# Kernel optimization log

Measured on AMD Instinct MI355X. Metric: run time of the kernel, lower is better.

The kernel has to match this reference:

```python
import jax, jax.numpy as jnp
import numpy as np

N_NODES = 50000
N_EDGES = 800000
HIDDEN = 256
LAYERS = 10


def setup_inputs() -> dict:
    key = jax.random.key(0)
    ks = jax.random.split(key, 8)
    x = jax.random.normal(ks[0], (N_NODES, 1), dtype=jnp.float32)
    edge_index = jax.random.randint(ks[1], (2, N_EDGES), 0, N_NODES, dtype=jnp.int64)
    # GCNConv weights (Glorot-ish scale)
    W1 = jax.random.normal(ks[2], (1, HIDDEN), dtype=jnp.float32) * (1.0 / np.sqrt(1))
    b1 = jnp.zeros((HIDDEN,), dtype=jnp.float32)
    W = jax.random.normal(ks[3], (HIDDEN, HIDDEN), dtype=jnp.float32) * (1.0 / np.sqrt(HIDDEN))
    b = jnp.zeros((HIDDEN,), dtype=jnp.float32)
    Wc = jax.random.normal(ks[4], (HIDDEN, 1), dtype=jnp.float32) * (1.0 / np.sqrt(HIDDEN))
    bc = jnp.zeros((1,), dtype=jnp.float32)
    return {"x": x, "edge_index": edge_index, "W1": W1, "b1": b1,
            "W": W, "b": b, "Wc": Wc, "bc": bc}


def _gcn_norm(edge_index, n_nodes):
    # PyG GCNConv default: add self-loops, symmetric normalization
    loop = jnp.arange(n_nodes, dtype=edge_index.dtype)
    src = jnp.concatenate([edge_index[0], loop])
    dst = jnp.concatenate([edge_index[1], loop])
    ones = jnp.ones(src.shape[0], dtype=jnp.float32)
    deg = jax.ops.segment_sum(ones, dst, num_segments=n_nodes)
    dinv = jnp.where(deg > 0, jax.lax.rsqrt(deg), 0.0)
    norm = dinv[src] * dinv[dst]  # [E+N]
    return src, dst, norm


def _gcn_conv(h, W, b, src, dst, norm, n_nodes):
    h = h @ W                                   # [N, H] dense transform first (small GEMM)
    msg = h[src] * norm[:, None]                # gather + scale  [E+N, H]
    out = jax.ops.segment_sum(msg, dst, num_segments=n_nodes)  # scatter-add
    return out + b


def reference(x, edge_index, W1, b1, W, b, Wc, bc):
    n = x.shape[0]
    src, dst, norm = _gcn_norm(edge_index, n)  # graph is static across layers
    h = jax.nn.relu(_gcn_conv(x, W1, b1, src, dst, norm, n))
    for _ in range(1, LAYERS):  # layers 1..9 share the same weights (self.conv reused)
        h = jax.nn.relu(_gcn_conv(h, W, b, src, dst, norm, n))
    return h @ Wc + bc  # [N, 1]
```

## Files before the change

### kernel.cpp

```cpp
#include <hip/hip_runtime.h>

typedef long long ll;
typedef __attribute__((ext_vector_type(8))) short short8;
typedef __attribute__((ext_vector_type(4))) float f32x4;
constexpr int HID = 256;
constexpr int LDSS = 264;

__device__ inline ushort f2bf(float f){
  uint u = __float_as_uint(f);
  u += 0x7FFFu + ((u >> 16) & 1u);
  return (ushort)(u >> 16);
}

__device__ inline int pinv(int q){ return (q & ~63) | ((q & 3)*16 + ((q >> 2) & 15)); }

__global__ void k_diag(float* out, int n, float val){
  int i = blockIdx.x*256 + threadIdx.x;
  if (i < n) out[i] = val;
}

__global__ void k_detect(const int* ei, int* flag){
  __shared__ int bad;
  if (threadIdx.x == 0) bad = 0;
  __syncthreads();
  for (int i = threadIdx.x; i < 2048; i += 256)
    if (ei[2*i+1] != 0) bad = 1;
  __syncthreads();
  if (threadIdx.x == 0) *flag = bad ? 0 : 1;
}

__global__ void k_count(const int* ei, ll E, const int* flag, int* cnt){
  ll i = (ll)blockIdx.x*256 + threadIdx.x;
  if (i >= E) return;
  int f = *flag;
  int d = f ? (int)((const ll*)ei)[E + i] : ei[E + i];
  atomicAdd(&cnt[d], 1);
}

__global__ void k_scan_a(const int* __restrict__ cnt, int* __restrict__ bsum, int n){
  __shared__ int s[256];
  int t = threadIdx.x, i = blockIdx.x*256 + t;
  s[t] = (i < n) ? cnt[i] : 0;
  __syncthreads();
  for (int off = 128; off; off >>= 1){
    if (t < off) s[t] += s[t + off];
    __syncthreads();
  }
  if (t == 0) bsum[blockIdx.x] = s[0];
}

__global__ void k_scan_b(const int* __restrict__ bsum, int* __restrict__ boff,
                         int nb, int* __restrict__ row_ptr, int n){
  __shared__ int s[256];
  int t = threadIdx.x;
  int v = (t < nb) ? bsum[t] : 0;
  s[t] = v; __syncthreads();
  for (int off = 1; off < 256; off <<= 1){
    int add = (t >= off) ? s[t - off] : 0;
    __syncthreads();
    s[t] += add;
    __syncthreads();
  }
  if (t < nb) boff[t] = s[t] - v;
  if (t == nb - 1) row_ptr[n] = s[t];
}

__global__ void k_scan_c(const int* __restrict__ cnt, const int* __restrict__ boff,
                         int* __restrict__ row_ptr, const float* __restrict__ x,
                         float* __restrict__ dinv, float* __restrict__ xd, int n){
  __shared__ int s[256];
  int t = threadIdx.x, i = blockIdx.x*256 + t;
  int v = (i < n) ? cnt[i] : 0;
  s[t] = v; __syncthreads();
  for (int off = 1; off < 256; off <<= 1){
    int add = (t >= off) ? s[t - off] : 0;
    __syncthreads();
    s[t] += add;
    __syncthreads();
  }
  if (i < n){
    row_ptr[i] = boff[blockIdx.x] + s[t] - v;
    float dv = 1.0f / sqrtf((float)(v + 1));
    dinv[i] = dv;
    xd[i] = x[i] * dv;
  }
}

__global__ void k_place(const int* ei, ll E, const int* flag, int* fill, int* col){
  ll i = (ll)blockIdx.x*256 + threadIdx.x;
  if (i >= E) return;
  int f = *flag;
  int s, d;
  if (f){ const ll* e64 = (const ll*)ei; s = (int)e64[i]; d = (int)e64[E + i]; }
  else  { s = ei[i]; d = ei[E + i]; }
  int p = atomicAdd(&fill[d], 1);
  col[p] = s;
}

__global__ void k_layer1(const float* __restrict__ xd, const int* __restrict__ row_ptr,
                         const int* __restrict__ col, float* __restrict__ g, int n){
  int i = blockIdx.x*256 + threadIdx.x;
  if (i >= n) return;
  float s = xd[i];
  int e0 = row_ptr[i], e1 = row_ptr[i+1];
  for (int e = e0; e < e1; ++e) s += xd[col[e]];
  g[i] = s;
}

__global__ void k_prep(const float* __restrict__ W, short* __restrict__ Bt,
                       const float* b1, const float* W1, const float* bm, const float* Wc,
                       float* b1_p, float* W1_p, float* bm_p, float* Wc_p){
  int idx = blockIdx.x*256 + threadIdx.x;
  if (idx < 16*8*64){
    int nb = idx >> 9, kc = (idx >> 6) & 7, l = idx & 63;
    short8 hi;
    #pragma unroll
    for (int j = 0; j < 8; ++j){
      int k = pinv(kc*32 + ((l >> 4) * 8) + j);
      int c = nb*16 + (l & 15);
      hi[j] = (short)f2bf(W[k*HID + c]);
    }
    ((short8*)Bt)[idx] = hi;
  } else if (blockIdx.x == 32){
    int q = threadIdx.x;
    int c = pinv(q);
    b1_p[q] = b1[c];
    W1_p[q] = W1[c];
    bm_p[q] = bm[c];
    Wc_p[q] = Wc[c];
  }
}

template<int MODE>
__global__ __launch_bounds__(256, 4) void k_gemm_mfma(
  const void* __restrict__ Ain, const short* __restrict__ Bt,
  const float* __restrict__ bias, const float* __restrict__ W1,
  const float* __restrict__ dinv, ushort* __restrict__ ts_bf, int n)
{
  __shared__ short Ah[64*LDSS];
  int t = threadIdx.x;
  int r0 = blockIdx.x * 64;

  #pragma unroll
  for (int i = 0; i < 8; ++i){
    int id  = i*256 + t;
    int row = id >> 5;
    int c16 = id & 31;
    int v   = r0 + row;
    short8 hi8 = {0,0,0,0,0,0,0,0};
    if (v < n){
      if (MODE == 0){
        float gv = dinv[v] * ((const float*)Ain)[v];
        const float4* wp = (const float4*)(W1 + c16*8);
        const float4* bp = (const float4*)(bias + c16*8);
        float4 w0 = wp[0], w1 = wp[1], b0 = bp[0], b1 = bp[1];
        hi8[0] = (short)f2bf(fmaxf(fmaf(gv,w0.x,b0.x), 0.f));
        hi8[1] = (short)f2bf(fmaxf(fmaf(gv,w0.y,b0.y), 0.f));
        hi8[2] = (short)f2bf(fmaxf(fmaf(gv,w0.z,b0.z), 0.f));
        hi8[3] = (short)f2bf(fmaxf(fmaf(gv,w0.w,b0.w), 0.f));
        hi8[4] = (short)f2bf(fmaxf(fmaf(gv,w1.x,b1.x), 0.f));
        hi8[5] = (short)f2bf(fmaxf(fmaf(gv,w1.y,b1.y), 0.f));
        hi8[6] = (short)f2bf(fmaxf(fmaf(gv,w1.z,b1.z), 0.f));
        hi8[7] = (short)f2bf(fmaxf(fmaf(gv,w1.w,b1.w), 0.f));
      } else {
        hi8 = ((const short8*)Ain)[(size_t)v*32 + c16];
      }
    }
    *(short8*)&Ah[row*LDSS + c16*8] = hi8;
  }
  __syncthreads();

  int l = t & 63, w = t >> 6;
  const short8* Btv = (const short8*)Bt;
  f32x4 acc[4][4];
  #pragma unroll
  for (int m = 0; m < 4; ++m)
    #pragma unroll
    for (int nf = 0; nf < 4; ++nf)
      acc[m][nf] = (f32x4){0.f,0.f,0.f,0.f};

  for (int kc = 0; kc < 8; ++kc){
    short8 ah[4];
    #pragma unroll
    for (int m = 0; m < 4; ++m){
      int row = m*16 + (l & 15);
      ah[m] = *(const short8*)&Ah[row*LDSS + (kc*4 + (l >> 4))*8];
    }
    #pragma unroll
    for (int nf = 0; nf < 4; ++nf){
      int nb = w*4 + nf;
      short8 bh = Btv[(size_t)(nb*8 + kc)*64 + l];
      #pragma unroll
      for (int m = 0; m < 4; ++m){
        acc[m][nf] = __builtin_amdgcn_mfma_f32_16x16x32_bf16(ah[m], bh, acc[m][nf], 0,0,0);
      }
    }
  }

  #pragma unroll
  for (int m = 0; m < 4; ++m){
    #pragma unroll
    for (int r = 0; r < 4; ++r){
      int v = r0 + m*16 + ((l >> 4)*4) + r;
      if (v < n){
        float dv = dinv[v];
        uint2 o;
        o.x = (uint)f2bf(dv * acc[m][0][r]) | ((uint)f2bf(dv * acc[m][1][r]) << 16);
        o.y = (uint)f2bf(dv * acc[m][2][r]) | ((uint)f2bf(dv * acc[m][3][r]) << 16);
        *(uint2*)((char*)ts_bf + (size_t)v*512 + w*128 + (l & 15)*8) = o;
      }
    }
  }
}

__device__ inline void bfacc(uint2 u, float4& a){
  a.x += __uint_as_float(u.x << 16);
  a.y += __uint_as_float(u.x & 0xFFFF0000u);
  a.z += __uint_as_float(u.y << 16);
  a.w += __uint_as_float(u.y & 0xFFFF0000u);
}

template<int LAST>
__global__ __launch_bounds__(256, 4) void k_scatter_bf(
  const ushort* __restrict__ ts_bf, const int* __restrict__ row_ptr,
  const int* __restrict__ col, const float* __restrict__ bias,
  const float* __restrict__ dinv, ushort* __restrict__ Abf,
  const float* __restrict__ Wc, const float* __restrict__ bc,
  float* __restrict__ out, int n)
{
  int w = (int)((blockIdx.x*256 + threadIdx.x) >> 6);
  int lane = threadIdx.x & 63;
  if (w >= n) return;
  const uint2* tsp = ((const uint2*)ts_bf) + lane;
  int e0 = row_ptr[w], e1 = row_ptr[w+1];

  float4 a0 = make_float4(0.f,0.f,0.f,0.f);
  float4 a1 = make_float4(0.f,0.f,0.f,0.f);
  float4 a2 = make_float4(0.f,0.f,0.f,0.f);
  float4 a3 = make_float4(0.f,0.f,0.f,0.f);
  bfacc(tsp[(size_t)w*64], a0);

  int e = e0;
  for (; e + 4 <= e1; e += 4){
    int c0 = __builtin_nontemporal_load(col + e + 0);
    int c1 = __builtin_nontemporal_load(col + e + 1);
    int c2 = __builtin_nontemporal_load(col + e + 2);
    int c3 = __builtin_nontemporal_load(col + e + 3);
    uint2 v0 = tsp[(size_t)c0*64];
    uint2 v1 = tsp[(size_t)c1*64];
    uint2 v2 = tsp[(size_t)c2*64];
    uint2 v3 = tsp[(size_t)c3*64];
    bfacc(v0, a0); bfacc(v1, a1); bfacc(v2, a2); bfacc(v3, a3);
  }
  for (; e < e1; ++e){
    uint2 v = tsp[(size_t)__builtin_nontemporal_load(col + e)*64];
    bfacc(v, a0);
  }

  a0.x += a1.x + a2.x + a3.x;
  a0.y += a1.y + a2.y + a3.y;
  a0.z += a1.z + a2.z + a3.z;
  a0.w += a1.w + a2.w + a3.w;

  float dv = dinv[w];
  float4 bb = ((const float4*)bias)[lane];
  if (LAST == 0){
    uint2 o;
    o.x = (uint)f2bf(fmaxf(fmaf(dv, a0.x, bb.x), 0.f))
        | ((uint)f2bf(fmaxf(fmaf(dv, a0.y, bb.y), 0.f)) << 16);
    o.y = (uint)f2bf(fmaxf(fmaf(dv, a0.z, bb.z), 0.f))
        | ((uint)f2bf(fmaxf(fmaf(dv, a0.w, bb.w), 0.f)) << 16);
    ((uint2*)Abf)[(size_t)w*64 + lane] = o;
  } else {
    float4 wc = ((const float4*)Wc)[lane];
    float s = fmaxf(fmaf(dv, a0.x, bb.x), 0.f)*wc.x
            + fmaxf(fmaf(dv, a0.y, bb.y), 0.f)*wc.y
            + fmaxf(fmaf(dv, a0.z, bb.z), 0.f)*wc.z
            + fmaxf(fmaf(dv, a0.w, bb.w), 0.f)*wc.w;
    #pragma unroll
    for (int off = 32; off; off >>= 1) s += __shfl_down(s, off, 64);
    if (lane == 0) out[w] = s + bc[0];
  }
}

extern "C" void kernel_launch(void* const* d_in, const int* in_sizes, int n_in,
                              void* d_out, int out_size, void* d_ws, size_t ws_size,
                              hipStream_t stream)
{
  const float* x  = (const float*)d_in[0];
  const int*   ei = (const int*)d_in[1];
  const float* W1 = (const float*)d_in[2];
  const float* b1 = (const float*)d_in[3];
  const float* Wm = (const float*)d_in[4];
  const float* bm = (const float*)d_in[5];
  const float* Wc = (const float*)d_in[6];
  const float* bc = (const float*)d_in[7];
  float* out = (float*)d_out;
  const int N = in_sizes[0];
  const ll  E = in_sizes[1] / 2;

  char* ws = (char*)d_ws;
  size_t off = 0;
  auto carve = [&](size_t bytes)->char*{
    char* p = ws + off; off += (bytes + 255) & ~(size_t)255; return p;
  };
  int*   cnt     = (int*)  carve((size_t)N*4);
  int*   row_ptr = (int*)  carve((size_t)(N+1)*4);
  int*   fill    = (int*)  carve((size_t)N*4);
  float* dinv    = (float*)carve((size_t)N*4);
  float* xd      = (float*)carve((size_t)N*4);
  float* g       = (float*)carve((size_t)N*4);
  int*   flag    = (int*)  carve(256);
  int*   bsum    = (int*)  carve(1024);
  int*   boff    = (int*)  carve(1024);
  float* b1_p    = (float*)carve(1024);
  float* W1_p    = (float*)carve(1024);
  float* bm_p    = (float*)carve(1024);
  float* Wc_p    = (float*)carve(1024);
  short* Bt      = (short*)carve((size_t)8192*8*2);
  int*   col     = (int*)  carve((size_t)E*4);
  ushort* ts_bf  = (ushort*)carve((size_t)N*HID*2);
  ushort* Abf    = (ushort*)carve((size_t)N*HID*2);
  if (off > ws_size){
    k_diag<<<(out_size+255)/256, 256, 0, stream>>>(out, out_size, (float)(ws_size >> 20));
    return;
  }

  hipMemsetAsync(cnt, 0, (size_t)N*4, stream);
  k_detect<<<1, 256, 0, stream>>>(ei, flag);
  int eblocks = (int)((E + 255) / 256);
  k_count<<<eblocks, 256, 0, stream>>>(ei, E, flag, cnt);
  int nb = (N + 255) / 256;
  k_scan_a<<<nb, 256, 0, stream>>>(cnt, bsum, N);
  k_scan_b<<<1, 256, 0, stream>>>(bsum, boff, nb, row_ptr, N);
  k_scan_c<<<nb, 256, 0, stream>>>(cnt, boff, row_ptr, x, dinv, xd, N);
  hipMemcpyAsync(fill, row_ptr, (size_t)N*4, hipMemcpyDeviceToDevice, stream);
  k_place<<<eblocks, 256, 0, stream>>>(ei, E, flag, fill, col);
  k_prep<<<33, 256, 0, stream>>>(Wm, Bt, b1, W1, bm, Wc, b1_p, W1_p, bm_p, Wc_p);
  k_layer1<<<(N+255)/256, 256, 0, stream>>>(xd, row_ptr, col, g, N);

  int gblocks = (N + 63) / 64;
  int sblocks = (N + 3) / 4;
  k_gemm_mfma<0><<<gblocks, 256, 0, stream>>>(g, Bt, b1_p, W1_p, dinv, ts_bf, N);
  k_scatter_bf<0><<<sblocks, 256, 0, stream>>>(ts_bf, row_ptr, col, bm_p, dinv, Abf, Wc_p, bc, out, N);
  for (int l = 0; l < 7; ++l){
    k_gemm_mfma<1><<<gblocks, 256, 0, stream>>>(Abf, Bt, bm_p, nullptr, dinv, ts_bf, N);
    k_scatter_bf<0><<<sblocks, 256, 0, stream>>>(ts_bf, row_ptr, col, bm_p, dinv, Abf, Wc_p, bc, out, N);
  }
  k_gemm_mfma<1><<<gblocks, 256, 0, stream>>>(Abf, Bt, bm_p, nullptr, dinv, ts_bf, N);
  k_scatter_bf<1><<<sblocks, 256, 0, stream>>>(ts_bf, row_ptr, col, bm_p, dinv, Abf, Wc_p, bc, out, N);
}
```

Measured before the change: 845.0 us.

## Load GEMM A tiles directly into LDS with XOR-swizzled layout

Result: slower. 974.4 us (+15.3%).

```diff
diff --git a/kernel.cpp b/kernel.cpp
--- a/kernel.cpp
+++ b/kernel.cpp
@@ -3,8 +3,9 @@
 typedef long long ll;
 typedef __attribute__((ext_vector_type(8))) short short8;
 typedef __attribute__((ext_vector_type(4))) float f32x4;
+typedef const __attribute__((address_space(1))) unsigned int gu32;
+typedef __attribute__((address_space(3))) unsigned int lu32;
 constexpr int HID = 256;
-constexpr int LDSS = 264;
 
 __device__ inline ushort f2bf(float f){
   uint u = __float_as_uint(f);
@@ -66,7 +67,8 @@
 }
 
 __global__ void k_scan_c(const int* __restrict__ cnt, const int* __restrict__ boff,
-                         int* __restrict__ row_ptr, const float* __restrict__ x,
+                         int* __restrict__ row_ptr, int* __restrict__ fill,
+                         const float* __restrict__ x,
                          float* __restrict__ dinv, float* __restrict__ xd, int n){
   __shared__ int s[256];
   int t = threadIdx.x, i = blockIdx.x*256 + t;
@@ -79,7 +81,9 @@
     __syncthreads();
   }
   if (i < n){
-    row_ptr[i] = boff[blockIdx.x] + s[t] - v;
+    int rp = boff[blockIdx.x] + s[t] - v;
+    row_ptr[i] = rp;
+    fill[i] = rp;
     float dv = 1.0f / sqrtf((float)(v + 1));
     dinv[i] = dv;
     xd[i] = x[i] * dv;
@@ -132,24 +136,32 @@
 }
 
 template<int MODE>
-__global__ __launch_bounds__(256, 4) void k_gemm_mfma(
+__global__ __launch_bounds__(256, 5) void k_gemm_mfma(
   const void* __restrict__ Ain, const short* __restrict__ Bt,
   const float* __restrict__ bias, const float* __restrict__ W1,
   const float* __restrict__ dinv, ushort* __restrict__ ts_bf, int n)
 {
-  __shared__ short Ah[64*LDSS];
+  __shared__ short Ah[64*256];
   int t = threadIdx.x;
+  int l = t & 63, w = t >> 6;
   int r0 = blockIdx.x * 64;
 
-  #pragma unroll
-  for (int i = 0; i < 8; ++i){
-    int id  = i*256 + t;
-    int row = id >> 5;
-    int c16 = id & 31;
-    int v   = r0 + row;
-    short8 hi8 = {0,0,0,0,0,0,0,0};
-    if (v < n){
-      if (MODE == 0){
+  if (MODE == 1){
+    const char* src = (const char*)Ain + (size_t)r0*512 + w*1024 + l*16;
+    #pragma unroll
+    for (int i = 0; i < 8; ++i){
+      __builtin_amdgcn_global_load_lds((gu32*)(src + (size_t)i*4096),
+                                       (lu32*)(Ah + i*2048 + w*512), 16, 0, 0);
+    }
+  } else {
+    #pragma unroll
+    for (int i = 0; i < 8; ++i){
+      int id  = i*256 + t;
+      int row = id >> 5;
+      int c16 = id & 31;
+      int v   = r0 + row;
+      short8 hi8 = {0,0,0,0,0,0,0,0};
+      if (v < n){
         float gv = dinv[v] * ((const float*)Ain)[v];
         const float4* wp = (const float4*)(W1 + c16*8);
         const float4* bp = (const float4*)(bias + c16*8);
@@ -162,15 +174,12 @@
         hi8[5] = (short)f2bf(fmaxf(fmaf(gv,w1.y,b1.y), 0.f));
         hi8[6] = (short)f2bf(fmaxf(fmaf(gv,w1.z,b1.z), 0.f));
         hi8[7] = (short)f2bf(fmaxf(fmaf(gv,w1.w,b1.w), 0.f));
-      } else {
-        hi8 = ((const short8*)Ain)[(size_t)v*32 + c16];
       }
-    }
-    *(short8*)&Ah[row*LDSS + c16*8] = hi8;
+      *(short8*)&Ah[row*256 + ((c16 ^ (row & 7)) * 8)] = hi8;
+    }
   }
   __syncthreads();
 
-  int l = t & 63, w = t >> 6;
   const short8* Btv = (const short8*)Bt;
   f32x4 acc[4][4];
   #pragma unroll
@@ -181,10 +190,11 @@
 
   for (int kc = 0; kc < 8; ++kc){
     short8 ah[4];
+    int chunk = kc*4 + (l >> 4);
     #pragma unroll
     for (int m = 0; m < 4; ++m){
       int row = m*16 + (l & 15);
-      ah[m] = *(const short8*)&Ah[row*LDSS + (kc*4 + (l >> 4))*8];
+      ah[m] = *(const short8*)&Ah[row*256 + ((chunk ^ (row & 7)) * 8)];
     }
     #pragma unroll
     for (int nf = 0; nf < 4; ++nf){
@@ -270,7 +280,8 @@
         | ((uint)f2bf(fmaxf(fmaf(dv, a0.y, bb.y), 0.f)) << 16);
     o.y = (uint)f2bf(fmaxf(fmaf(dv, a0.z, bb.z), 0.f))
         | ((uint)f2bf(fmaxf(fmaf(dv, a0.w, bb.w), 0.f)) << 16);
-    ((uint2*)Abf)[(size_t)w*64 + lane] = o;
+    int c = lane >> 1, h = lane & 1;
+    *(uint2*)((char*)Abf + (size_t)w*512 + (((c ^ (w & 7)) << 4) | (h << 3))) = o;
   } else {
     float4 wc = ((const float4*)Wc)[lane];
     float s = fmaxf(fmaf(dv, a0.x, bb.x), 0.f)*wc.x
@@ -320,7 +331,7 @@
   short* Bt      = (short*)carve((size_t)8192*8*2);
   int*   col     = (int*)  carve((size_t)E*4);
   ushort* ts_bf  = (ushort*)carve((size_t)N*HID*2);
-  ushort* Abf    = (ushort*)carve((size_t)N*HID*2);
+  ushort* Abf    = (ushort*)carve((size_t)N*HID*2 + 64*512);
   if (off > ws_size){
     k_diag<<<(out_size+255)/256, 256, 0, stream>>>(out, out_size, (float)(ws_size >> 20));
     return;
@@ -333,8 +344,7 @@
   int nb = (N + 255) / 256;
   k_scan_a<<<nb, 256, 0, stream>>>(cnt, bsum, N);
   k_scan_b<<<1, 256, 0, stream>>>(bsum, boff, nb, row_ptr, N);
-  k_scan_c<<<nb, 256, 0, stream>>>(cnt, boff, row_ptr, x, dinv, xd, N);
-  hipMemcpyAsync(fill, row_ptr, (size_t)N*4, hipMemcpyDeviceToDevice, stream);
+  k_scan_c<<<nb, 256, 0, stream>>>(cnt, boff, row_ptr, fill, x, dinv, xd, N);
   k_place<<<eblocks, 256, 0, stream>>>(ei, E, flag, fill, col);
   k_prep<<<33, 256, 0, stream>>>(Wm, Bt, b1, W1, bm, Wc, b1_p, W1_p, bm_p, Wc_p);
   k_layer1<<<(N+255)/256, 256, 0, stream>>>(xd, row_ptr, col, g, N);
```
